# Performance work log

Hardware: AMD Instinct MI355X
Metric: run time of the kernel (lower is better)

The kernel has to match this reference:

```python
import jax, jax.numpy as jnp
import numpy as np

N_NODES = 50000
N_EDGES = 800000
HID = 128
IMG_D = 2048
TXT_D = 768


def setup_inputs() -> dict:
    key = jax.random.key(0)
    ks = jax.random.split(key, 20)
    rn = lambda k, sh, s=0.02: (jax.random.normal(k, sh, jnp.float32) * s)
    inp = {
        "node_id": jax.random.randint(ks[0], (N_NODES,), 0, N_NODES),
        "img_h": jax.random.normal(ks[1], (N_NODES, IMG_D), jnp.float32),
        "txt_h": jax.random.normal(ks[2], (N_NODES, TXT_D), jnp.float32),
        "src": jax.random.randint(ks[3], (N_EDGES,), 0, N_NODES),
        "dst": jax.random.randint(ks[4], (N_EDGES,), 0, N_NODES),
        # parameters
        "emb_table": rn(ks[5], (N_NODES, HID)),
        "W_img": rn(ks[6], (IMG_D, HID)),
        "img_W1": rn(ks[7], (2 * HID, HID)), "img_b1": jnp.zeros((HID,), jnp.float32),
        "img_W2": rn(ks[8], (HID, HID)),     "img_b2": jnp.zeros((HID,), jnp.float32),
        "img_W3": rn(ks[9], (HID, 1)),       "img_b3": jnp.zeros((1,), jnp.float32),
        "W_txt": rn(ks[10], (TXT_D, HID)),
        "txt_W1": rn(ks[11], (2 * HID, HID)), "txt_b1": jnp.zeros((HID,), jnp.float32),
        "txt_W2": rn(ks[12], (HID, HID)),      "txt_b2": jnp.zeros((HID,), jnp.float32),
        "txt_W3": rn(ks[13], (HID, 1)),        "txt_b3": jnp.zeros((1,), jnp.float32),
        "comb_W": rn(ks[14], (2 * HID, HID)),  "comb_b": jnp.zeros((HID,), jnp.float32),
        "fc_W": rn(ks[15], (HID, HID)),
        "attn_a": rn(ks[16], (2 * HID,)),
    }
    return inp


def _gate_mlp(x, W1, b1, W2, b2, W3, b3):
    # Linear->ReLU->Linear->ReLU->Linear->Sigmoid, output [N,1]
    h = jax.nn.relu(x @ W1 + b1)
    h = jax.nn.relu(h @ W2 + b2)
    return jax.nn.sigmoid(h @ W3 + b3)


def reference(node_id, img_h, txt_h, src, dst, emb_table, W_img,
              img_W1, img_b1, img_W2, img_b2, img_W3, img_b3,
              W_txt, txt_W1, txt_b1, txt_W2, txt_b2, txt_W3, txt_b3,
              comb_W, comb_b, fc_W, attn_a):
    N = node_id.shape[0]
    H = fc_W.shape[0]
    # use_emb=True path: h = embedding lookup; embed = h.detach()
    embed = jax.lax.stop_gradient(emb_table[node_id])  # [N,H]
    # gated image branch
    img_f = img_h @ W_img                                             # [N,H]
    g_img = _gate_mlp(jnp.concatenate([embed, img_f], 1),
                      img_W1, img_b1, img_W2, img_b2, img_W3, img_b3)  # [N,1]
    img_v = g_img * img_f + (1.0 - g_img) * embed
    # gated text branch
    txt_f = txt_h @ W_txt
    g_txt = _gate_mlp(jnp.concatenate([embed, txt_f], 1),
                      txt_W1, txt_b1, txt_W2, txt_b2, txt_W3, txt_b3)
    txt_v = g_txt * txt_f + (1.0 - g_txt) * embed
    # combined gate (plain Linear, vector-valued gate)
    gate = jnp.concatenate([img_v, txt_v], 1) @ comb_W + comb_b       # [N,H]
    h = gate * img_v + (1.0 - gate) * txt_v
    # GAT projection
    z = h @ fc_W                                                      # [N,H]
    # edge attention: leaky_relu(a^T [z_src ; z_dst]) without materializing [E,2H]
    a1, a2 = attn_a[:H], attn_a[H:]
    e_src = z @ a1                                                    # [N]
    e_dst = z @ a2
    e = jax.nn.leaky_relu(e_src[src] + e_dst[dst], 0.01)              # [E]
    # segment softmax over incoming edges of each dst node
    emax = jax.ops.segment_max(e, dst, num_segments=N)
    emax = jnp.where(jnp.isfinite(emax), emax, 0.0)
    ex = jnp.exp(e - emax[dst])
    denom = jax.ops.segment_sum(ex, dst, num_segments=N)
    alpha = ex / jnp.maximum(denom[dst], 1e-20)                       # [E]
    # weighted scatter-sum of source features
    h_out = jax.ops.segment_sum(alpha[:, None] * z[src], dst, num_segments=N)
    return h_out
```

## Files before the change

### kernel.cpp

```cpp
#include <hip/hip_runtime.h>
#include <hip/hip_bf16.h>

#define N_NODES 50000
#define N_EDGES 800000
#define HID     128
#define IMG_D   2048
#define TXT_D   768
#define EPB     16

typedef short          s16x8 __attribute__((ext_vector_type(8)));
typedef unsigned short u16x8 __attribute__((ext_vector_type(8)));
typedef unsigned short u16x4 __attribute__((ext_vector_type(4)));
typedef float          f32x4 __attribute__((ext_vector_type(4)));

static __device__ __forceinline__ unsigned short f2bf(float f) {
    unsigned int x = __float_as_uint(f);
    x += 0x7fffu + ((x >> 16) & 1u);
    return (unsigned short)(x >> 16);
}
struct BfPair { unsigned short h, l; };
static __device__ __forceinline__ BfPair bsplit(float a) {
    BfPair p;
    p.h = f2bf(a);
    float hf = __uint_as_float((unsigned int)p.h << 16);
    p.l = f2bf(a - hf);
    return p;
}

static __device__ __forceinline__ f32x4 mfma16(s16x8 a, s16x8 b, f32x4 c) {
    return __builtin_amdgcn_mfma_f32_16x16x32_bf16(a, b, c, 0, 0, 0);
}

#define WB_IMG  0u
#define WB_TXT  32768u
#define WB_IW1  45056u
#define WB_TW1  49152u
#define WB_COMB 53248u
#define WB_IW2  57344u
#define WB_TW2  59392u
#define WB_FC   61440u
#define W_TOTAL_ELEMS 507904

__global__ __launch_bounds__(256)
void prep_all(const float* __restrict__ Wimg, const float* __restrict__ Wtxt,
              const float* __restrict__ iW1, const float* __restrict__ tW1,
              const float* __restrict__ combW, const float* __restrict__ iW2,
              const float* __restrict__ tW2, const float* __restrict__ fcW,
              unsigned short* __restrict__ Whi, unsigned short* __restrict__ Wlo) {
    int idx = blockIdx.x * 256 + threadIdx.x;
    if (idx >= W_TOTAL_ELEMS) return;
    const float* S; int li; size_t base;
    if (idx < 262144)      { S = Wimg;  li = idx;          base = 0; }
    else if (idx < 360448) { S = Wtxt;  li = idx - 262144; base = 262144; }
    else if (idx < 393216) { S = iW1;   li = idx - 360448; base = 360448; }
    else if (idx < 425984) { S = tW1;   li = idx - 393216; base = 393216; }
    else if (idx < 458752) { S = combW; li = idx - 425984; base = 425984; }
    else if (idx < 475136) { S = iW2;   li = idx - 458752; base = 458752; }
    else if (idx < 491520) { S = tW2;   li = idx - 475136; base = 475136; }
    else                   { S = fcW;   li = idx - 491520; base = 491520; }
    int k = li >> 7, col = li & 127;
    int kf = k >> 5, kr = k & 31, b = kr >> 3, i = kr & 7;
    int nf = col >> 4, rr = col & 15, l = (b << 4) | rr;
    size_t o = base + ((((size_t)kf * 8 + nf) * 64) + l) * 8 + i;
    BfPair p = bsplit(S[(size_t)k * HID + col]);
    Whi[o] = p.h; Wlo[o] = p.l;
}

static __device__ __forceinline__ void zacc(f32x4 acc[4][4]) {
    #pragma unroll
    for (int m = 0; m < 4; ++m)
        #pragma unroll
        for (int n = 0; n < 4; ++n) acc[m][n] = f32x4{0.f, 0.f, 0.f, 0.f};
}

static __device__ __forceinline__ void stash4(unsigned short* sHi, unsigned short* sLo,
                                              int r, int k, float4 v) {
    int e = (k & 64) | ((k & 63) ^ ((r & 7) << 3));
    BfPair p0 = bsplit(v.x), p1 = bsplit(v.y), p2 = bsplit(v.z), p3 = bsplit(v.w);
    u16x4 hh = {p0.h, p1.h, p2.h, p3.h}, ll = {p0.l, p1.l, p2.l, p3.l};
    *(u16x4*)&sHi[r * 128 + e] = hh;
    *(u16x4*)&sLo[r * 128 + e] = ll;
}
static __device__ __forceinline__ void stash1(unsigned short* sHi, unsigned short* sLo,
                                              int r, int k, float v) {
    int e = (k & 64) | ((k & 63) ^ ((r & 7) << 3));
    BfPair p = bsplit(v);
    sHi[r * 128 + e] = p.h;
    sLo[r * 128 + e] = p.l;
}

static __device__ __forceinline__ void gemm_chunks(
        f32x4 acc[4][4], const unsigned short* sHi, const unsigned short* sLo,
        const unsigned short* __restrict__ Whi, const unsigned short* __restrict__ Wlo,
        size_t wbase8, int kfbase, int lane, int wr, int wc) {
    #pragma unroll
    for (int c = 0; c < 2; ++c)
    #pragma unroll
    for (int ks = 0; ks < 2; ++ks) {
        s16x8 ah[4], al[4], bh[4], bl[4];
        const int kf = kfbase + (c << 1) + ks;
        const int eb = (ks << 5) | ((lane >> 4) << 3);
        #pragma unroll
        for (int m = 0; m < 4; ++m) {
            int r = (wr << 6) + (m << 4) + (lane & 15);
            int e = (c << 6) | (eb ^ ((r & 7) << 3));
            ah[m] = __builtin_bit_cast(s16x8, *(const u16x8*)&sHi[r * 128 + e]);
            al[m] = __builtin_bit_cast(s16x8, *(const u16x8*)&sLo[r * 128 + e]);
        }
        #pragma unroll
        for (int n = 0; n < 4; ++n) {
            size_t fo = wbase8 + ((size_t)kf * 8 + (wc << 2) + n) * 64 + lane;
            bh[n] = __builtin_bit_cast(s16x8, ((const u16x8*)Whi)[fo]);
            bl[n] = __builtin_bit_cast(s16x8, ((const u16x8*)Wlo)[fo]);
        }
        #pragma unroll
        for (int m = 0; m < 4; ++m)
        #pragma unroll
        for (int n = 0; n < 4; ++n) {
            acc[m][n] = mfma16(ah[m], bh[n], acc[m][n]);
            acc[m][n] = mfma16(al[m], bh[n], acc[m][n]);
            acc[m][n] = mfma16(ah[m], bl[n], acc[m][n]);
        }
    }
}

static __device__ __forceinline__ void rowdot_reduce(float vals[16], float* red,
                                                     int lane, int wr, int wc) {
    #pragma unroll
    for (int off = 1; off < 16; off <<= 1)
        #pragma unroll
        for (int t = 0; t < 16; ++t) vals[t] += __shfl_xor(vals[t], off, 64);
    if ((lane & 15) == 0) {
        int g = lane >> 4;
        #pragma unroll
        for (int m = 0; m < 4; ++m)
            #pragma unroll
            for (int jj = 0; jj < 4; ++jj)
                red[wc * 128 + (wr << 6) + (g << 2) + (m << 4) + jj] = vals[(m << 2) + jj];
    }
}

template<int K>
__global__ __launch_bounds__(256, 2)
void feat_gemm_mfma(const float* __restrict__ A,
                    const unsigned short* __restrict__ Bhi,
                    const unsigned short* __restrict__ Blo,
                    float* __restrict__ C, int M) {
    __shared__ __align__(16) unsigned short sAhi[128][64];
    __shared__ __align__(16) unsigned short sAlo[128][64];

    const int tid  = threadIdx.x;
    const int lane = tid & 63;
    const int wid  = tid >> 6;
    const int wr   = wid >> 1;
    const int wc   = wid & 1;
    const int row0 = blockIdx.x * 128;

    f32x4 acc[4][4];
    zacc(acc);

    for (int k0 = 0; k0 < K; k0 += 64) {
        #pragma unroll
        for (int it = 0; it < 8; ++it) {
            int chunk = tid + (it << 8);
            int r  = chunk >> 4;
            int kc = chunk & 15;
            int gr = row0 + r; if (gr >= M) gr = M - 1;
            const float4 av = *(const float4*)&A[(size_t)gr * K + k0 + (kc << 2)];
            BfPair p0 = bsplit(av.x), p1 = bsplit(av.y), p2 = bsplit(av.z), p3 = bsplit(av.w);
            u16x4 h = {p0.h, p1.h, p2.h, p3.h};
            u16x4 l = {p0.l, p1.l, p2.l, p3.l};
            int e = (kc << 2) ^ ((r & 7) << 3);
            *(u16x4*)&sAhi[r][e] = h;
            *(u16x4*)&sAlo[r][e] = l;
        }
        __syncthreads();

        #pragma unroll
        for (int ks = 0; ks < 2; ++ks) {
            s16x8 ah[4], al[4], bh[4], bl[4];
            const int e0 = (ks << 5) | ((lane >> 4) << 3);
            #pragma unroll
            for (int m = 0; m < 4; ++m) {
                int r = (wr << 6) + (m << 4) + (lane & 15);
                int e = e0 ^ ((r & 7) << 3);
                ah[m] = __builtin_bit_cast(s16x8, *(const u16x8*)&sAhi[r][e]);
                al[m] = __builtin_bit_cast(s16x8, *(const u16x8*)&sAlo[r][e]);
            }
            const int kf = (k0 >> 5) + ks;
            #pragma unroll
            for (int n = 0; n < 4; ++n) {
                int nf = (wc << 2) + n;
                size_t fo = ((size_t)kf * 8 + nf) * 64 + lane;
                bh[n] = __builtin_bit_cast(s16x8, ((const u16x8*)Bhi)[fo]);
                bl[n] = __builtin_bit_cast(s16x8, ((const u16x8*)Blo)[fo]);
            }
            #pragma unroll
            for (int m = 0; m < 4; ++m)
                #pragma unroll
                for (int n = 0; n < 4; ++n) {
                    acc[m][n] = mfma16(ah[m], bh[n], acc[m][n]);
                    acc[m][n] = mfma16(al[m], bh[n], acc[m][n]);
                    acc[m][n] = mfma16(ah[m], bl[n], acc[m][n]);
                }
        }
        __syncthreads();
    }

    const int crow = (wr << 6) + ((lane >> 4) << 2);
    const int ccol = (wc << 6) + (lane & 15);
    #pragma unroll
    for (int m = 0; m < 4; ++m)
        #pragma unroll
        for (int n = 0; n < 4; ++n)
            #pragma unroll
            for (int j = 0; j < 4; ++j) {
                int grow = row0 + crow + (m << 4) + j;
                if (grow < M) C[(size_t)grow * HID + ccol + (n << 4)] = acc[m][n][j];
            }
}

__global__ __launch_bounds__(256, 2)
void node_mfma(const int* __restrict__ node_id, const float* __restrict__ emb_table,
               const float* __restrict__ img_f_all, const float* __restrict__ txt_f_all,
               const unsigned short* __restrict__ Whi, const unsigned short* __restrict__ Wlo,
               const float* __restrict__ ib1, const float* __restrict__ ib2,
               const float* __restrict__ iW3, const float* __restrict__ ib3,
               const float* __restrict__ tb1, const float* __restrict__ tb2,
               const float* __restrict__ tW3, const float* __restrict__ tb3,
               const float* __restrict__ combb, const float* __restrict__ attn,
               float* __restrict__ z_out, float* __restrict__ e_src, float* __restrict__ e_dst,
               int M) {
    __shared__ __align__(16) unsigned short sHi[128 * 128];
    __shared__ __align__(16) unsigned short sLo[128 * 128];
    __shared__ int   sNid[128];
    __shared__ float sGi[128], sGt[128];
    __shared__ float red[4 * 128];

    const int tid = threadIdx.x, lane = tid & 63, wid = tid >> 6;
    const int wr = wid >> 1, wc = wid & 1;
    const int n0 = blockIdx.x * 128;
    const int crow = (wr << 6) + ((lane >> 4) << 2);
    const int ccol = (wc << 6) + (lane & 15);

    if (tid < 128) { int gr = n0 + tid; if (gr >= M) gr = M - 1; sNid[tid] = node_id[gr]; }
    __syncthreads();

    f32x4 acc[4][4];

    auto stage_emb = [&]() {
        #pragma unroll
        for (int it = 0; it < 16; ++it) {
            int chunk = tid + (it << 8);
            int r = chunk >> 5, k = (chunk & 31) << 2;
            float4 v = *(const float4*)&emb_table[(size_t)sNid[r] * HID + k];
            stash4(sHi, sLo, r, k, v);
        }
    };
    auto stage_row = [&](const float* __restrict__ src) {
        #pragma unroll
        for (int it = 0; it < 16; ++it) {
            int chunk = tid + (it << 8);
            int r = chunk >> 5, k = (chunk & 31) << 2;
            int grow = n0 + r; if (grow >= M) grow = M - 1;
            float4 v = *(const float4*)&src[(size_t)grow * HID + k];
            stash4(sHi, sLo, r, k, v);
        }
    };
    auto stage_fused = [&](const float* __restrict__ src, const float* g) {
        #pragma unroll
        for (int it = 0; it < 16; ++it) {
            int chunk = tid + (it << 8);
            int r = chunk >> 5, k = (chunk & 31) << 2;
            int grow = n0 + r; if (grow >= M) grow = M - 1;
            float gg = g[r];
            float4 f = *(const float4*)&src[(size_t)grow * HID + k];
            float4 e = *(const float4*)&emb_table[(size_t)sNid[r] * HID + k];
            float4 v;
            v.x = gg * f.x + (1.f - gg) * e.x;
            v.y = gg * f.y + (1.f - gg) * e.y;
            v.z = gg * f.z + (1.f - gg) * e.z;
            v.w = gg * f.w + (1.f - gg) * e.w;
            stash4(sHi, sLo, r, k, v);
        }
    };
    auto gate_tail = [&](size_t wb2, const float* __restrict__ b2,
                         const float* __restrict__ W3, const float* __restrict__ b3,
                         float* g) {
        zacc(acc);
        gemm_chunks(acc, sHi, sLo, Whi, Wlo, wb2, 0, lane, wr, wc);
        float bv[4], wv[4];
        #pragma unroll
        for (int n = 0; n < 4; ++n) { bv[n] = b2[ccol + (n << 4)]; wv[n] = W3[ccol + (n << 4)]; }
        float vals[16];
        #pragma unroll
        for (int m = 0; m < 4; ++m)
            #pragma unroll
            for (int jj = 0; jj < 4; ++jj) {
                float s = 0.f;
                #pragma unroll
                for (int n = 0; n < 4; ++n)
                    s += fmaxf(acc[m][n][jj] + bv[n], 0.f) * wv[n];
                vals[(m << 2) + jj] = s;
            }
        rowdot_reduce(vals, red, lane, wr, wc);
        __syncthreads();
        if (tid < 128) g[tid] = 1.f / (1.f + expf(-(red[tid] + red[128 + tid] + b3[0])));
        __syncthreads();
    };
    auto gate_mlp = [&](const float* __restrict__ feat, size_t wb1,
                        const float* __restrict__ b1, size_t wb2,
                        const float* __restrict__ b2, const float* __restrict__ W3,
                        const float* __restrict__ b3, float* g) {
        zacc(acc);
        stage_emb();  __syncthreads();
        gemm_chunks(acc, sHi, sLo, Whi, Wlo, wb1, 0, lane, wr, wc);
        __syncthreads();
        stage_row(feat);  __syncthreads();
        gemm_chunks(acc, sHi, sLo, Whi, Wlo, wb1, 4, lane, wr, wc);
        __syncthreads();
        float bv[4];
        #pragma unroll
        for (int n = 0; n < 4; ++n) bv[n] = b1[ccol + (n << 4)];
        #pragma unroll
        for (int m = 0; m < 4; ++m)
            #pragma unroll
            for (int jj = 0; jj < 4; ++jj) {
                int r = crow + (m << 4) + jj;
                #pragma unroll
                for (int n = 0; n < 4; ++n)
                    stash1(sHi, sLo, r, ccol + (n << 4), fmaxf(acc[m][n][jj] + bv[n], 0.f));
            }
        __syncthreads();
        gate_tail(wb2, b2, W3, b3, g);
    };

    gate_mlp(img_f_all, WB_IW1, ib1, WB_IW2, ib2, iW3, ib3, sGi);
    gate_mlp(txt_f_all, WB_TW1, tb1, WB_TW2, tb2, tW3, tb3, sGt);

    zacc(acc);
    stage_fused(img_f_all, sGi);  __syncthreads();
    gemm_chunks(acc, sHi, sLo, Whi, Wlo, WB_COMB, 0, lane, wr, wc);
    __syncthreads();
    stage_fused(txt_f_all, sGt);  __syncthreads();
    gemm_chunks(acc, sHi, sLo, Whi, Wlo, WB_COMB, 4, lane, wr, wc);
    __syncthreads();

    {
        float bv[4];
        #pragma unroll
        for (int n = 0; n < 4; ++n) bv[n] = combb[ccol + (n << 4)];
        #pragma unroll
        for (int m = 0; m < 4; ++m)
            #pragma unroll
            for (int jj = 0; jj < 4; ++jj) {
                int r = crow + (m << 4) + jj;
                int grow = n0 + r; if (grow >= M) grow = M - 1;
                float gi = sGi[r], gt = sGt[r];
                size_t ebase = (size_t)sNid[r] * HID;
                #pragma unroll
                for (int n = 0; n < 4; ++n) {
                    int c = ccol + (n << 4);
                    float em = emb_table[ebase + c];
                    float fi = img_f_all[(size_t)grow * HID + c];
                    float ft = txt_f_all[(size_t)grow * HID + c];
                    float iv = gi * fi + (1.f - gi) * em;
                    float tv = gt * ft + (1.f - gt) * em;
                    float gate = acc[m][n][jj] + bv[n];
                    stash1(sHi, sLo, r, c, gate * iv + (1.f - gate) * tv);
                }
            }
    }
    __syncthreads();

    zacc(acc);
    gemm_chunks(acc, sHi, sLo, Whi, Wlo, WB_FC, 0, lane, wr, wc);
    {
        float a1v[4], a2v[4];
        #pragma unroll
        for (int n = 0; n < 4; ++n) {
            a1v[n] = attn[ccol + (n << 4)];
            a2v[n] = attn[HID + ccol + (n << 4)];
        }
        float v1[16], v2[16];
        #pragma unroll
        for (int m = 0; m < 4; ++m)
            #pragma unroll
            for (int jj = 0; jj < 4; ++jj) {
                int grow = n0 + crow + (m << 4) + jj;
                float s1 = 0.f, s2 = 0.f;
                #pragma unroll
                for (int n = 0; n < 4; ++n) {
                    float zv = acc[m][n][jj];
                    if (grow < M) z_out[(size_t)grow * HID + ccol + (n << 4)] = zv;
                    s1 += zv * a1v[n];
                    s2 += zv * a2v[n];
                }
                v1[(m << 2) + jj] = s1;
                v2[(m << 2) + jj] = s2;
            }
        rowdot_reduce(v1, red, lane, wr, wc);
        rowdot_reduce(v2, red + 256, lane, wr, wc);
    }
    __syncthreads();
    if (tid < 128) {
        int gr = n0 + tid;
        if (gr < M) {
            e_src[gr] = red[tid] + red[128 + tid];
            e_dst[gr] = red[256 + tid] + red[384 + tid];
        }
    }
}

__global__ __launch_bounds__(256)
void edge_softmax_pre(const int* __restrict__ src, const int* __restrict__ dst,
                      const float* __restrict__ e_src, const float* __restrict__ e_dst,
                      float* __restrict__ exbuf, float* __restrict__ denom) {
    int k = blockIdx.x * 256 + threadIdx.x;
    if (k >= N_EDGES) return;
    float e = e_src[src[k]] + e_dst[dst[k]];
    e = (e >= 0.f) ? e : 0.01f * e;
    float ex = expf(e);
    exbuf[k] = ex;
    atomicAdd(&denom[dst[k]], ex);
}

__global__ __launch_bounds__(128)
void edge_aggregate(const int* __restrict__ src, const int* __restrict__ dst,
                    const float* __restrict__ exbuf, const float* __restrict__ denom,
                    const float* __restrict__ z, float* __restrict__ hout) {
    int j = threadIdx.x;
    int base = blockIdx.x * EPB;
    int end = base + EPB;
    if (end > N_EDGES) end = N_EDGES;
    for (int k = base; k < end; ++k) {
        int d = dst[k], s = src[k];
        float alpha = exbuf[k] / fmaxf(denom[d], 1e-20f);
        atomicAdd(&hout[(size_t)d * HID + j], alpha * z[(size_t)s * HID + j]);
    }
}

extern "C" void kernel_launch(void* const* d_in, const int* in_sizes, int n_in,
                              void* d_out, int out_size, void* d_ws, size_t ws_size,
                              hipStream_t stream) {
    const int*   node_id = (const int*)d_in[0];
    const float* img_h   = (const float*)d_in[1];
    const float* txt_h   = (const float*)d_in[2];
    const int*   src     = (const int*)d_in[3];
    const int*   dst     = (const int*)d_in[4];
    const float* emb     = (const float*)d_in[5];
    const float* W_img   = (const float*)d_in[6];
    const float* iW1     = (const float*)d_in[7];
    const float* ib1     = (const float*)d_in[8];
    const float* iW2     = (const float*)d_in[9];
    const float* ib2     = (const float*)d_in[10];
    const float* iW3     = (const float*)d_in[11];
    const float* ib3     = (const float*)d_in[12];
    const float* W_txt   = (const float*)d_in[13];
    const float* tW1     = (const float*)d_in[14];
    const float* tb1     = (const float*)d_in[15];
    const float* tW2     = (const float*)d_in[16];
    const float* tb2     = (const float*)d_in[17];
    const float* tW3     = (const float*)d_in[18];
    const float* tb3     = (const float*)d_in[19];
    const float* combW   = (const float*)d_in[20];
    const float* combb   = (const float*)d_in[21];
    const float* fcW     = (const float*)d_in[22];
    const float* attn    = (const float*)d_in[23];

    float* ws    = (float*)d_ws;
    float* img_f = ws;
    float* txt_f = img_f + (size_t)N_NODES * HID;
    float* e_s   = txt_f + (size_t)N_NODES * HID;
    float* e_d   = e_s + N_NODES;
    float* denom = e_d + N_NODES;
    float* exbuf = denom + N_NODES;
    float* z     = img_f;

    unsigned short* Whi = (unsigned short*)exbuf;
    unsigned short* Wlo = Whi + W_TOTAL_ELEMS;

    float* out_f = (float*)d_out;
    hipMemsetAsync(denom, 0, (size_t)N_NODES * sizeof(float), stream);
    hipMemsetAsync(out_f, 0, (size_t)N_NODES * HID * sizeof(float), stream);

    prep_all<<<W_TOTAL_ELEMS / 256, 256, 0, stream>>>(W_img, W_txt, iW1, tW1, combW,
                                                      iW2, tW2, fcW, Whi, Wlo);

    feat_gemm_mfma<IMG_D><<<(N_NODES + 127) / 128, 256, 0, stream>>>(
        img_h, Whi + WB_IMG * 8, Wlo + WB_IMG * 8, img_f, N_NODES);
    feat_gemm_mfma<TXT_D><<<(N_NODES + 127) / 128, 256, 0, stream>>>(
        txt_h, Whi + WB_TXT * 8, Wlo + WB_TXT * 8, txt_f, N_NODES);

    node_mfma<<<(N_NODES + 127) / 128, 256, 0, stream>>>(
        node_id, emb, img_f, txt_f, Whi, Wlo,
        ib1, ib2, iW3, ib3, tb1, tb2, tW3, tb3,
        combb, attn, z, e_s, e_d, N_NODES);

    edge_softmax_pre<<<(N_EDGES + 255) / 256, 256, 0, stream>>>(src, dst, e_s, e_d, exbuf, denom);

    edge_aggregate<<<(N_EDGES + EPB - 1) / EPB, 128, 0, stream>>>(src, dst, exbuf, denom, z, out_f);
}
```

Measured before the change: 1.321 ms.

## Replace atomic edge scatter with CSR bucketing and per-node gather aggregation

Builds a dst-sorted CSR of source indices with a histogram, a single-block prefix scan and an atomic bucket scatter. A single per-destination-node kernel then computes the leaky-relu exp weights, their sum and the weighted feature sum in registers, with one wavefront per node. This removes the per-feature float atomics into the output, the exbuf/denom buffers and the output memset. The cost is three extra small launches, a serial single-block scan, and edge order within a node that is not deterministic, which can change floating-point summation order.

Result: faster. 1.191 ms (-9.8%).

```diff
diff --git a/kernel.cpp b/kernel.cpp
--- a/kernel.cpp
+++ b/kernel.cpp
@@ -6,7 +6,6 @@
 #define HID     128
 #define IMG_D   2048
 #define TXT_D   768
-#define EPB     16
 
 typedef short          s16x8 __attribute__((ext_vector_type(8)));
 typedef unsigned short u16x8 __attribute__((ext_vector_type(8)));
@@ -413,31 +412,65 @@
 }
 
 __global__ __launch_bounds__(256)
-void edge_softmax_pre(const int* __restrict__ src, const int* __restrict__ dst,
-                      const float* __restrict__ e_src, const float* __restrict__ e_dst,
-                      float* __restrict__ exbuf, float* __restrict__ denom) {
+void edge_hist(const int* __restrict__ dst, int* __restrict__ cnt) {
+    int k = blockIdx.x * 256 + threadIdx.x;
+    if (k < N_EDGES) atomicAdd(&cnt[dst[k]], 1);
+}
+
+__global__ __launch_bounds__(1024)
+void scan_offsets(int* __restrict__ cnt) {
+    __shared__ int part[1024];
+    int tid = threadIdx.x;
+    const int CH = (N_NODES + 1023) / 1024;
+    int base = tid * CH;
+    int lim = base + CH; if (lim > N_NODES) lim = N_NODES;
+    int sum = 0;
+    for (int i = base; i < lim; ++i) sum += cnt[i];
+    part[tid] = sum;
+    __syncthreads();
+    for (int off = 1; off < 1024; off <<= 1) {
+        int v = (tid >= off) ? part[tid - off] : 0;
+        __syncthreads();
+        part[tid] += v;
+        __syncthreads();
+    }
+    int run = part[tid] - sum;
+    for (int i = base; i < lim; ++i) { int c = cnt[i]; cnt[i] = run; run += c; }
+}
+
+__global__ __launch_bounds__(256)
+void edge_scatter(const int* __restrict__ src, const int* __restrict__ dst,
+                  int* __restrict__ offs, int* __restrict__ bucket) {
     int k = blockIdx.x * 256 + threadIdx.x;
     if (k >= N_EDGES) return;
-    float e = e_src[src[k]] + e_dst[dst[k]];
-    e = (e >= 0.f) ? e : 0.01f * e;
-    float ex = expf(e);
-    exbuf[k] = ex;
-    atomicAdd(&denom[dst[k]], ex);
-}
-
-__global__ __launch_bounds__(128)
-void edge_aggregate(const int* __restrict__ src, const int* __restrict__ dst,
-                    const float* __restrict__ exbuf, const float* __restrict__ denom,
-                    const float* __restrict__ z, float* __restrict__ hout) {
-    int j = threadIdx.x;
-    int base = blockIdx.x * EPB;
-    int end = base + EPB;
-    if (end > N_EDGES) end = N_EDGES;
-    for (int k = base; k < end; ++k) {
-        int d = dst[k], s = src[k];
-        float alpha = exbuf[k] / fmaxf(denom[d], 1e-20f);
-        atomicAdd(&hout[(size_t)d * HID + j], alpha * z[(size_t)s * HID + j]);
-    }
+    int pos = atomicAdd(&offs[dst[k]], 1);
+    bucket[pos] = src[k];
+}
+
+__global__ __launch_bounds__(256)
+void edge_aggregate_csr(const int* __restrict__ bucket, const int* __restrict__ offs,
+                        const float* __restrict__ e_src, const float* __restrict__ e_dst,
+                        const float* __restrict__ z, float* __restrict__ hout) {
+    int d = blockIdx.x * 4 + (threadIdx.x >> 6);
+    if (d >= N_NODES) return;
+    int lane = threadIdx.x & 63;
+    int start = (d == 0) ? 0 : offs[d - 1];
+    int end = offs[d];
+    float edv = e_dst[d];
+    float ax = 0.f, ay = 0.f, S = 0.f;
+    for (int k = start; k < end; ++k) {
+        int s = bucket[k];
+        float e = e_src[s] + edv;
+        e = (e >= 0.f) ? e : 0.01f * e;
+        float ex = expf(e);
+        S += ex;
+        const float2 zv = *(const float2*)&z[(size_t)s * HID + (lane << 1)];
+        ax += ex * zv.x;
+        ay += ex * zv.y;
+    }
+    float inv = 1.f / fmaxf(S, 1e-20f);
+    float2 o; o.x = ax * inv; o.y = ay * inv;
+    *(float2*)&hout[(size_t)d * HID + (lane << 1)] = o;
 }
 
 extern "C" void kernel_launch(void* const* d_in, const int* in_sizes, int n_in,
@@ -473,19 +506,20 @@
     float* txt_f = img_f + (size_t)N_NODES * HID;
     float* e_s   = txt_f + (size_t)N_NODES * HID;
     float* e_d   = e_s + N_NODES;
-    float* denom = e_d + N_NODES;
-    float* exbuf = denom + N_NODES;
+    int*   cnt   = (int*)(e_d + N_NODES);
+    int*   bucket= cnt + N_NODES;
     float* z     = img_f;
 
-    unsigned short* Whi = (unsigned short*)exbuf;
+    unsigned short* Whi = (unsigned short*)bucket;
     unsigned short* Wlo = Whi + W_TOTAL_ELEMS;
 
     float* out_f = (float*)d_out;
-    hipMemsetAsync(denom, 0, (size_t)N_NODES * sizeof(float), stream);
-    hipMemsetAsync(out_f, 0, (size_t)N_NODES * HID * sizeof(float), stream);
+    hipMemsetAsync(cnt, 0, (size_t)N_NODES * sizeof(int), stream);
 
     prep_all<<<W_TOTAL_ELEMS / 256, 256, 0, stream>>>(W_img, W_txt, iW1, tW1, combW,
                                                       iW2, tW2, fcW, Whi, Wlo);
+    edge_hist<<<(N_EDGES + 255) / 256, 256, 0, stream>>>(dst, cnt);
+    scan_offsets<<<1, 1024, 0, stream>>>(cnt);
 
     feat_gemm_mfma<IMG_D><<<(N_NODES + 127) / 128, 256, 0, stream>>>(
         img_h, Whi + WB_IMG * 8, Wlo + WB_IMG * 8, img_f, N_NODES);
@@ -497,7 +531,7 @@
         ib1, ib2, iW3, ib3, tb1, tb2, tW3, tb3,
         combb, attn, z, e_s, e_d, N_NODES);
 
-    edge_softmax_pre<<<(N_EDGES + 255) / 256, 256, 0, stream>>>(src, dst, e_s, e_d, exbuf, denom);
-
-    edge_aggregate<<<(N_EDGES + EPB - 1) / EPB, 128, 0, stream>>>(src, dst, exbuf, denom, z, out_f);
-}
+    edge_scatter<<<(N_EDGES + 255) / 256, 256, 0, stream>>>(src, dst, cnt, bucket);
+
+    edge_aggregate_csr<<<(N_NODES + 3) / 4, 256, 0, stream>>>(bucket, cnt, e_s, e_d, z, out_f);
+}
```
